# Optimization experiments

Hardware: AMD Instinct MI355X
Metric: run time of the kernel (lower is better)

The kernel has to match this reference:

```python
import jax, jax.numpy as jnp
import numpy as np
import math

B, S, H, NH = 2, 2048, 2048, 16
HD = H // NH  # 128
NEG = -1e9


def setup_inputs() -> dict:
    key = jax.random.key(0)
    ks = jax.random.split(key, 6)
    x = jax.random.normal(ks[0], (B, S, H), dtype=jnp.float32)
    # realistic rotary frequencies: cos/sin interleaved, shape [S, HD//2, 2]
    inv_freq = 1.0 / (10000.0 ** (np.arange(0, HD, 2, dtype=np.float32) / HD))
    t = np.arange(S, dtype=np.float32)
    ang = np.outer(t, inv_freq)  # [S, HD//2]
    freqs_cis = jnp.asarray(np.stack([np.cos(ang), np.sin(ang)], axis=-1), dtype=jnp.float32)
    # additive causal mask [1,1,S,S]
    causal = jnp.triu(jnp.full((S, S), NEG, dtype=jnp.float32), k=1)[None, None]
    scale = 0.02
    wq = jax.random.normal(ks[1], (H, H), dtype=jnp.float32) * scale
    wk = jax.random.normal(ks[2], (H, H), dtype=jnp.float32) * scale
    wv = jax.random.normal(ks[3], (H, H), dtype=jnp.float32) * scale
    wo = jax.random.normal(ks[4], (H, H), dtype=jnp.float32) * scale
    position_ids = jnp.broadcast_to(jnp.arange(S, dtype=jnp.int64)[None, :], (B, S))
    return {"x": x, "freqs_cis": freqs_cis, "attention_mask": causal,
            "wq": wq, "wk": wk, "wv": wv, "wo": wo, "position_ids": position_ids}


def _apply_rotary(t, freqs):
    # t: [B,S,NH,HD], freqs: [B,S,1,HD//2,2]
    b, s, nh, hd = t.shape
    tp = t.reshape(b, s, nh, hd // 2, 2)
    tr, ti = tp[..., 0], tp[..., 1]
    fr, fi = freqs[..., 0], freqs[..., 1]
    out = jnp.stack([tr * fr - ti * fi, tr * fi + ti * fr], axis=-1)
    return out.reshape(b, s, nh, hd)


def reference(x, freqs_cis, attention_mask, wq, wk, wv, wo, position_ids):
    b, s, h = x.shape
    q = (x @ wq.T).reshape(b, s, NH, HD)
    k = (x @ wk.T).reshape(b, s, NH, HD)
    v = (x @ wv.T).reshape(b, s, NH, HD)
    freqs = freqs_cis[position_ids][:, :, None]  # [B,S,1,HD//2,2]
    q = _apply_rotary(q, freqs)
    k = _apply_rotary(k, freqs)
    # [B,NH,S,HD]
    q = q.transpose(0, 2, 1, 3)
    k = k.transpose(0, 2, 1, 3)
    v = v.transpose(0, 2, 1, 3)
    scores = jnp.einsum('bhqd,bhkd->bhqk', q, k) / math.sqrt(HD)
    scores = scores + attention_mask
    attn = jax.nn.softmax(scores, axis=-1)
    out = jnp.einsum('bhqk,bhkd->bhqd', attn, v)
    out = out.transpose(0, 2, 1, 3).reshape(b, s, h)
    return out @ wo.T
```

## Files before the change

### kernel.cpp

```cpp
#include <hip/hip_runtime.h>

#define DEVI __device__ __forceinline__

typedef unsigned short u16;
typedef unsigned int   u32;
typedef __attribute__((ext_vector_type(4))) float f32x4;
typedef __attribute__((ext_vector_type(8))) short short8;
typedef __attribute__((ext_vector_type(8))) __bf16 bf16x8;

#define B_   2
#define S_   2048
#define H_   2048
#define NH_  16
#define HD_  128
#define BH_  (B_*NH_)
#define QSCALE 0.12751743f

DEVI u16 f2b(float f){
  u32 u = __builtin_bit_cast(u32, f);
  u32 r = (u + 0x7fffu + ((u >> 16) & 1u)) >> 16;
  return (u16)r;
}
DEVI float b2f(u16 h){
  u32 u = ((u32)h) << 16;
  return __builtin_bit_cast(float, u);
}
DEVI u32 cvt_pk_bf16(float lo, float hi){
  u32 r; asm("v_cvt_pk_bf16_f32 %0, %1, %2" : "=v"(r) : "v"(lo), "v"(hi)); return r;
}
DEVI f32x4 mfma_bf16(short8 a, short8 b, f32x4 c){
  return __builtin_amdgcn_mfma_f32_16x16x32_bf16(
      __builtin_bit_cast(bf16x8, a), __builtin_bit_cast(bf16x8, b), c, 0, 0, 0);
}
DEVI void gl_lds16(const void* g, void* l){
  __builtin_amdgcn_global_load_lds((const __attribute__((address_space(1))) void*)g,
                                   (__attribute__((address_space(3))) void*)l, 16, 0, 0);
}

template<int LOG2CPR>
DEVI void stage_swz(const u16* __restrict__ src, int srcStride , u16* lds, int tid){
  const int wid = tid >> 6, lane = tid & 63;
#pragma unroll
  for (int i = 0; i < 4; ++i){
    int lin = i*256 + wid*64 + lane;
    int row = lin >> LOG2CPR;
    int cb  = ((lin & ((1 << LOG2CPR) - 1)) * 16) ^ ((row & 7) << 4);
    gl_lds16(src + (size_t)row * srcStride + (cb >> 1),
             lds + (size_t)(i*256 + wid*64) * 8);
  }
}

__global__ __launch_bounds__(256) void cvt5_kernel(
    const float* __restrict__ x,  const float* __restrict__ wq,
    const float* __restrict__ wk, const float* __restrict__ wv,
    const float* __restrict__ wo, u16* __restrict__ xb,
    u16* __restrict__ wqkv, u16* __restrict__ wob){
  int i = blockIdx.x * 256 + threadIdx.x;
  const float* src; u16* dst; int off;
  if      (i < 2097152){ src = x;  dst = xb;             off = i;           }
  else if (i < 3145728){ src = wq; dst = wqkv;           off = i - 2097152; }
  else if (i < 4194304){ src = wk; dst = wqkv + 4194304; off = i - 3145728; }
  else if (i < 5242880){ src = wv; dst = wqkv + 8388608; off = i - 4194304; }
  else                 { src = wo; dst = wob;            off = i - 5242880; }
  float4 v = ((const float4*)src)[off];
  uint2 o;
  o.x = (u32)f2b(v.x) | ((u32)f2b(v.y) << 16);
  o.y = (u32)f2b(v.z) | ((u32)f2b(v.w) << 16);
  ((uint2*)dst)[off] = o;
}

template<int EPI>
__global__ __launch_bounds__(256) void gemm_bt(
    const u16* __restrict__ A, const u16* __restrict__ Bw,
    float* __restrict__ C, u16* __restrict__ Qd, u16* __restrict__ Kd, u16* __restrict__ Vd,
    int M, int N, int K)
{
  __shared__ __align__(16) u16 As[128*64];
  __shared__ __align__(16) u16 Bs[128*64];
  const int tid  = threadIdx.x, lane = tid & 63, wid = tid >> 6;
  const int wr   = wid >> 1, wc = wid & 1;
  const int lrow = lane & 15, lk = lane >> 4;
  const int RB = blockIdx.y * 128, CB = blockIdx.x * 128;
  f32x4 acc[4][4] = {};

  for (int k0 = 0; k0 < K; k0 += 64){
    __syncthreads();
    stage_swz<3>(A  + (size_t)RB * K + k0, K, As, tid);
    stage_swz<3>(Bw + (size_t)CB * K + k0, K, Bs, tid);
    __syncthreads();
#pragma unroll
    for (int kk = 0; kk < 2; ++kk){
      short8 af[4], bf[4];
#pragma unroll
      for (int m = 0; m < 4; ++m){
        int row = wr*64 + m*16 + lrow;
        int cb  = (kk*64 + lk*16) ^ ((row & 7) << 4);
        af[m] = *(const short8*)&As[row*64 + (cb >> 1)];
      }
#pragma unroll
      for (int n = 0; n < 4; ++n){
        int row = wc*64 + n*16 + lrow;
        int cb  = (kk*64 + lk*16) ^ ((row & 7) << 4);
        bf[n] = *(const short8*)&Bs[row*64 + (cb >> 1)];
      }
#pragma unroll
      for (int m = 0; m < 4; ++m)
#pragma unroll
        for (int n = 0; n < 4; ++n)
          acc[m][n] = mfma_bf16(af[m], bf[n], acc[m][n]);
    }
  }

#pragma unroll
  for (int m = 0; m < 4; ++m){
#pragma unroll
    for (int n = 0; n < 4; ++n){
#pragma unroll
      for (int r = 0; r < 4; ++r){
        int row = RB + wr*64 + m*16 + lk*4 + r;
        int col = CB + wc*64 + n*16 + lrow;
        float v = acc[m][n][r];
        if constexpr (EPI == 0){
          C[(size_t)row * N + col] = v;
        } else {
          int which = col >> 11;
          int hd = col & 2047;
          int h = hd >> 7, d = hd & 127;
          int b = row >> 11, s = row & 2047;
          u16* dst = (which == 0) ? Qd : (which == 1) ? Kd : Vd;
          dst[(((size_t)(b*NH_ + h)) * S_ + s) * HD_ + d] = f2b(v);
        }
      }
    }
  }
}

__global__ __launch_bounds__(256) void rope_kernel(u16* __restrict__ Q, u16* __restrict__ K,
                                                   const float* __restrict__ F){
  int idx = blockIdx.x * 256 + threadIdx.x;
  int d2 = idx & 63;
  int s  = (idx >> 6) & (S_ - 1);
  int bh = idx >> 17;
  size_t off = ((size_t)bh * S_ + s) * HD_ + d2*2;
  float c = F[s*128 + d2*2], sn = F[s*128 + d2*2 + 1];
  u32 qp = *(const u32*)(Q + off);
  float tr = b2f((u16)qp), ti = b2f((u16)(qp >> 16));
  float q0 = (tr*c - ti*sn) * QSCALE, q1 = (tr*sn + ti*c) * QSCALE;
  *(u32*)(Q + off) = (u32)f2b(q0) | ((u32)f2b(q1) << 16);
  u32 kp = *(const u32*)(K + off);
  tr = b2f((u16)kp); ti = b2f((u16)(kp >> 16));
  float k0 = tr*c - ti*sn, k1 = tr*sn + ti*c;
  *(u32*)(K + off) = (u32)f2b(k0) | ((u32)f2b(k1) << 16);
}

__global__ void transpose_v(const u16* __restrict__ V, u16* __restrict__ Vt){
  __shared__ u16 t[32][33];
  int s0 = blockIdx.x * 32, d0 = blockIdx.y * 32, bh = blockIdx.z;
  const u16* vb = V  + (size_t)bh * S_ * HD_;
  u16*       tb = Vt + (size_t)bh * HD_ * S_;
  int tx = threadIdx.x, ty = threadIdx.y;
#pragma unroll
  for (int i = 0; i < 4; ++i)
    t[ty + i*8][tx] = vb[(size_t)(s0 + ty + i*8) * HD_ + d0 + tx];
  __syncthreads();
#pragma unroll
  for (int i = 0; i < 4; ++i)
    tb[(size_t)(d0 + ty + i*8) * S_ + s0 + tx] = t[tx][ty + i*8];
}

__global__ __launch_bounds__(256) void attn_kernel(
    const u16* __restrict__ Q, const u16* __restrict__ K, const u16* __restrict__ Vt,
    u16* __restrict__ O)
{
  __shared__ __align__(16) u16 Ks[2][64*128];
  __shared__ __align__(16) u16 Vs[2][128*64];
  __shared__ __align__(16) u16 Ps[4][16*64];
  const int tid  = threadIdx.x, lane = tid & 63, wid = tid >> 6;
  const int lrow = lane & 15, lk = lane >> 4;

  const int lin = blockIdx.x;
  const int bh  = (lin & 7) | ((lin >> 7) << 3);
  const int x   = (lin >> 3) & 15;

  const u16* Kb  = K  + (size_t)bh * S_ * HD_;
  const u16* Vtb = Vt + (size_t)bh * HD_ * S_;
  const int b = bh >> 4, h = bh & 15;
  u16* const pw = &Ps[wid][0];

  for (int pass = 0; pass < 2; ++pass){
    const int qb = pass ? x : (31 - x);
    const int q0 = qb * 64;
    const int ntile = qb + 1;
    const int qg = q0 + wid*16 + lrow;

    short8 qf[4];
    {
      const u16* qp_ = Q + ((size_t)bh * S_ + qg) * HD_;
#pragma unroll
      for (int kc = 0; kc < 4; ++kc) qf[kc] = *(const short8*)&qp_[kc*32 + lk*8];
    }

    f32x4 acco[8] = {};
    float m_ = -3.0e38f, l_ = 0.0f;

    int cur = 0;
    stage_swz<4>(Kb,  HD_, &Ks[0][0], tid);
    stage_swz<3>(Vtb, S_,  &Vs[0][0], tid);
    __syncthreads();

    for (int t = 0; t < ntile; ++t){
      if (t + 1 < ntile){
        stage_swz<4>(Kb  + (size_t)(t+1)*64*HD_, HD_, &Ks[cur^1][0], tid);
        stage_swz<3>(Vtb + (t+1)*64,             S_,  &Vs[cur^1][0], tid);
      }
      const int kv0 = t*64;
      const u16* ks = &Ks[cur][0];
      const u16* vs = &Vs[cur][0];

      f32x4 sc[4] = {};
      __builtin_amdgcn_s_setprio(1);
#pragma unroll
      for (int nt = 0; nt < 4; ++nt){
        int row = nt*16 + lrow;
#pragma unroll
        for (int kc = 0; kc < 4; ++kc){
          int cb = (kc*64 + lk*16) ^ ((row & 7) << 4);
          short8 kf = *(const short8*)&ks[row*128 + (cb >> 1)];
          sc[nt] = mfma_bf16(kf, qf[kc], sc[nt]);
        }
      }
      __builtin_amdgcn_s_setprio(0);

      if (t == ntile - 1){
#pragma unroll
        for (int nt = 0; nt < 4; ++nt)
#pragma unroll
          for (int r = 0; r < 4; ++r)
            if (kv0 + nt*16 + lk*4 + r > qg) sc[nt][r] = -1.0e30f;
      }

      {
        float pmax = sc[0][0];
#pragma unroll
        for (int nt = 0; nt < 4; ++nt)
#pragma unroll
          for (int r = 0; r < 4; ++r) pmax = fmaxf(pmax, sc[nt][r]);
        pmax = fmaxf(pmax, __shfl_xor(pmax, 16));
        pmax = fmaxf(pmax, __shfl_xor(pmax, 32));
        if (!__all(pmax - m_ <= 11.0f)){
          float mn = fmaxf(m_, pmax);
          float c = exp2f(m_ - mn);
          l_ *= c;
#pragma unroll
          for (int dt = 0; dt < 8; ++dt)
#pragma unroll
            for (int r = 0; r < 4; ++r) acco[dt][r] *= c;
          m_ = mn;
        }
        float rs = 0.0f;
#pragma unroll
        for (int nt = 0; nt < 4; ++nt)
#pragma unroll
          for (int r = 0; r < 4; ++r){
            float p = exp2f(sc[nt][r] - m_);
            sc[nt][r] = p;
            rs += p;
          }
        rs += __shfl_xor(rs, 16);
        rs += __shfl_xor(rs, 32);
        l_ += rs;
#pragma unroll
        for (int nt = 0; nt < 4; ++nt){
          uint2 wv;
          wv.x = cvt_pk_bf16(sc[nt][0], sc[nt][1]);
          wv.y = cvt_pk_bf16(sc[nt][2], sc[nt][3]);
          int boff = (nt*32 + lk*8) ^ ((lrow & 7) << 4);
          *(uint2*)((char*)&pw[lrow*64] + boff) = wv;
        }
      }

#pragma unroll
      for (int kc2 = 0; kc2 < 2; ++kc2){
        int pboff = (kc2*64 + lk*16) ^ ((lrow & 7) << 4);
        short8 pf = *(const short8*)((const char*)&pw[lrow*64] + pboff);
        __builtin_amdgcn_s_setprio(1);
#pragma unroll
        for (int dt = 0; dt < 8; ++dt){
          int row = dt*16 + lrow;
          int cb = (kc2*64 + lk*16) ^ ((row & 7) << 4);
          short8 vf = *(const short8*)&vs[row*64 + (cb >> 1)];
          acco[dt] = mfma_bf16(vf, pf, acco[dt]);
        }
        __builtin_amdgcn_s_setprio(0);
      }

      __syncthreads();
      cur ^= 1;
    }

    {
      float inv = 1.0f / l_;
      u16* ob = O + ((size_t)(b*S_ + qg)) * H_ + h*128;
#pragma unroll
      for (int dt = 0; dt < 8; ++dt){
        uint2 wv;
        wv.x = cvt_pk_bf16(acco[dt][0]*inv, acco[dt][1]*inv);
        wv.y = cvt_pk_bf16(acco[dt][2]*inv, acco[dt][3]*inv);
        *(uint2*)&ob[dt*16 + lk*4] = wv;
      }
    }
    __syncthreads();
  }
}

extern "C" void kernel_launch(void* const* d_in, const int* in_sizes, int n_in,
                              void* d_out, int out_size, void* d_ws, size_t ws_size,
                              hipStream_t stream)
{
  (void)in_sizes; (void)n_in; (void)out_size; (void)ws_size;
  const float* x  = (const float*)d_in[0];
  const float* fc = (const float*)d_in[1];
  const float* wq = (const float*)d_in[3];
  const float* wk = (const float*)d_in[4];
  const float* wv = (const float*)d_in[5];
  const float* wo = (const float*)d_in[6];

  char* w = (char*)d_ws;
  u16* xb   = (u16*)(w);
  u16* wqkv = (u16*)(w + 16777216);
  u16* wob  = (u16*)(w + 41943040);
  u16* Qr   = (u16*)(w + 50331648);
  u16* Kr   = (u16*)(w + 67108864);
  u16* Vr   = (u16*)(w + 83886080);
  u16* Vt   = (u16*)(w + 100663296);
  u16* aO   = (u16*)(w + 117440512);
  float* out = (float*)d_out;

  cvt5_kernel<<<24576, 256, 0, stream>>>(x, wq, wk, wv, wo, xb, wqkv, wob);

  gemm_bt<1><<<dim3(48, 32), 256, 0, stream>>>(xb, wqkv, nullptr, Qr, Kr, Vr, 4096, 6144, 2048);
  rope_kernel<<<16384, 256, 0, stream>>>(Qr, Kr, fc);
  transpose_v<<<dim3(64, 4, 32), dim3(32, 8), 0, stream>>>(Vr, Vt);
  attn_kernel<<<512, 256, 0, stream>>>(Qr, Kr, Vt, aO);
  gemm_bt<0><<<dim3(16, 32), 256, 0, stream>>>(aO, wob, out, nullptr, nullptr, nullptr, 4096, 2048, 2048);
}
```

Baseline: 275.5 us.

## Software-pipeline QK^T one tile ahead of softmax and PV in attention

Restructures the flash-attention loop so the QK^T scores for tile t+1 are computed while softmax and the PV product run on tile t. K and V staging are split, with V loaded after a mid-iteration barrier. Full __syncthreads is replaced by hand-written barriers with partial vmcnt waits so global loads can stay in flight. This aims to overlap MFMA and exp work and hide load latency, at the cost of more live registers and tight, fragile waitcnt assumptions about how many loads are outstanding.

```diff
diff --git a/kernel.cpp b/kernel.cpp
--- a/kernel.cpp
+++ b/kernel.cpp
@@ -168,6 +168,11 @@
     tb[(size_t)(d0 + ty + i*8) * S_ + s0 + tx] = t[tx][ty + i*8];
 }
 
+#define BAR_MID() do{ asm volatile("s_waitcnt lgkmcnt(0)" ::: "memory"); \
+                      __builtin_amdgcn_s_barrier(); } while(0)
+#define BAR_END() do{ asm volatile("s_waitcnt vmcnt(8) lgkmcnt(0)" ::: "memory"); \
+                      __builtin_amdgcn_s_barrier(); } while(0)
+
 __global__ __launch_bounds__(256) void attn_kernel(
     const u16* __restrict__ Q, const u16* __restrict__ K, const u16* __restrict__ Vt,
     u16* __restrict__ O)
@@ -201,50 +206,78 @@
     }
 
     f32x4 acco[8] = {};
+    f32x4 scp[4];
     float m_ = -3.0e38f, l_ = 0.0f;
 
-    int cur = 0;
     stage_swz<4>(Kb,  HD_, &Ks[0][0], tid);
     stage_swz<3>(Vtb, S_,  &Vs[0][0], tid);
     __syncthreads();
 
-    for (int t = 0; t < ntile; ++t){
-      if (t + 1 < ntile){
-        stage_swz<4>(Kb  + (size_t)(t+1)*64*HD_, HD_, &Ks[cur^1][0], tid);
-        stage_swz<3>(Vtb + (t+1)*64,             S_,  &Vs[cur^1][0], tid);
-      }
-      const int kv0 = t*64;
-      const u16* ks = &Ks[cur][0];
-      const u16* vs = &Vs[cur][0];
-
-      f32x4 sc[4] = {};
-      __builtin_amdgcn_s_setprio(1);
+    {
+      if (1 < ntile) stage_swz<4>(Kb + (size_t)64*HD_, HD_, &Ks[1][0], tid);
+      const u16* ks = &Ks[0][0];
 #pragma unroll
       for (int nt = 0; nt < 4; ++nt){
+        f32x4 a = {0.f,0.f,0.f,0.f};
         int row = nt*16 + lrow;
 #pragma unroll
         for (int kc = 0; kc < 4; ++kc){
           int cb = (kc*64 + lk*16) ^ ((row & 7) << 4);
           short8 kf = *(const short8*)&ks[row*128 + (cb >> 1)];
-          sc[nt] = mfma_bf16(kf, qf[kc], sc[nt]);
-        }
-      }
-      __builtin_amdgcn_s_setprio(0);
-
-      if (t == ntile - 1){
+          a = mfma_bf16(kf, qf[kc], a);
+        }
+        scp[nt] = a;
+      }
+      if (ntile == 1){
 #pragma unroll
         for (int nt = 0; nt < 4; ++nt)
 #pragma unroll
           for (int r = 0; r < 4; ++r)
-            if (kv0 + nt*16 + lk*4 + r > qg) sc[nt][r] = -1.0e30f;
+            if (nt*16 + lk*4 + r > qg) scp[nt][r] = -1.0e30f;
+      }
+      BAR_MID();
+      if (1 < ntile) stage_swz<3>(Vtb + 64, S_, &Vs[1][0], tid);
+      BAR_END();
+    }
+
+    for (int t = 1; t <= ntile; ++t){
+      const int cur = t & 1;
+      f32x4 scn[4];
+      if (t < ntile){
+        if (t + 1 < ntile) stage_swz<4>(Kb + (size_t)(t+1)*64*HD_, HD_, &Ks[cur^1][0], tid);
+        const u16* ks = &Ks[cur][0];
+        __builtin_amdgcn_s_setprio(1);
+#pragma unroll
+        for (int nt = 0; nt < 4; ++nt){
+          f32x4 a = {0.f,0.f,0.f,0.f};
+          int row = nt*16 + lrow;
+#pragma unroll
+          for (int kc = 0; kc < 4; ++kc){
+            int cb = (kc*64 + lk*16) ^ ((row & 7) << 4);
+            short8 kf = *(const short8*)&ks[row*128 + (cb >> 1)];
+            a = mfma_bf16(kf, qf[kc], a);
+          }
+          scn[nt] = a;
+        }
+        __builtin_amdgcn_s_setprio(0);
+        if (t == ntile - 1){
+          const int kv0 = t*64;
+#pragma unroll
+          for (int nt = 0; nt < 4; ++nt)
+#pragma unroll
+            for (int r = 0; r < 4; ++r)
+              if (kv0 + nt*16 + lk*4 + r > qg) scn[nt][r] = -1.0e30f;
+        }
+      } else {
+        asm volatile("s_waitcnt vmcnt(0)" ::: "memory");
       }
 
       {
-        float pmax = sc[0][0];
+        float pmax = scp[0][0];
 #pragma unroll
         for (int nt = 0; nt < 4; ++nt)
 #pragma unroll
-          for (int r = 0; r < 4; ++r) pmax = fmaxf(pmax, sc[nt][r]);
+          for (int r = 0; r < 4; ++r) pmax = fmaxf(pmax, scp[nt][r]);
         pmax = fmaxf(pmax, __shfl_xor(pmax, 16));
         pmax = fmaxf(pmax, __shfl_xor(pmax, 32));
         if (!__all(pmax - m_ <= 11.0f)){
@@ -262,8 +295,8 @@
         for (int nt = 0; nt < 4; ++nt)
 #pragma unroll
           for (int r = 0; r < 4; ++r){
-            float p = exp2f(sc[nt][r] - m_);
-            sc[nt][r] = p;
+            float p = exp2f(scp[nt][r] - m_);
+            scp[nt][r] = p;
             rs += p;
           }
         rs += __shfl_xor(rs, 16);
@@ -272,30 +305,38 @@
 #pragma unroll
         for (int nt = 0; nt < 4; ++nt){
           uint2 wv;
-          wv.x = cvt_pk_bf16(sc[nt][0], sc[nt][1]);
-          wv.y = cvt_pk_bf16(sc[nt][2], sc[nt][3]);
+          wv.x = cvt_pk_bf16(scp[nt][0], scp[nt][1]);
+          wv.y = cvt_pk_bf16(scp[nt][2], scp[nt][3]);
           int boff = (nt*32 + lk*8) ^ ((lrow & 7) << 4);
           *(uint2*)((char*)&pw[lrow*64] + boff) = wv;
         }
       }
 
-#pragma unroll
-      for (int kc2 = 0; kc2 < 2; ++kc2){
-        int pboff = (kc2*64 + lk*16) ^ ((lrow & 7) << 4);
-        short8 pf = *(const short8*)((const char*)&pw[lrow*64] + pboff);
-        __builtin_amdgcn_s_setprio(1);
-#pragma unroll
-        for (int dt = 0; dt < 8; ++dt){
-          int row = dt*16 + lrow;
-          int cb = (kc2*64 + lk*16) ^ ((row & 7) << 4);
-          short8 vf = *(const short8*)&vs[row*64 + (cb >> 1)];
-          acco[dt] = mfma_bf16(vf, pf, acco[dt]);
-        }
-        __builtin_amdgcn_s_setprio(0);
-      }
-
-      __syncthreads();
-      cur ^= 1;
+      {
+        const u16* vs = &Vs[cur^1][0];
+#pragma unroll
+        for (int kc2 = 0; kc2 < 2; ++kc2){
+          int pboff = (kc2*64 + lk*16) ^ ((lrow & 7) << 4);
+          short8 pf = *(const short8*)((const char*)&pw[lrow*64] + pboff);
+          __builtin_amdgcn_s_setprio(1);
+#pragma unroll
+          for (int dt = 0; dt < 8; ++dt){
+            int row = dt*16 + lrow;
+            int cb = (kc2*64 + lk*16) ^ ((row & 7) << 4);
+            short8 vf = *(const short8*)&vs[row*64 + (cb >> 1)];
+            acco[dt] = mfma_bf16(vf, pf, acco[dt]);
+          }
+          __builtin_amdgcn_s_setprio(0);
+        }
+      }
+
+      if (t < ntile){
+        BAR_MID();
+        if (t + 1 < ntile) stage_swz<3>(Vtb + (t+1)*64, S_, &Vs[cur^1][0], tid);
+#pragma unroll
+        for (int nt = 0; nt < 4; ++nt) scp[nt] = scn[nt];
+        BAR_END();
+      }
     }
 
     {
```

Measured after the change: 316.3 us. 1.15x slower.
